# Kernel tuning notes

Measured on AMD Instinct MI355X. Metric: run time of the kernel, lower is better.

The kernel has to match this reference:

```python
import jax, jax.numpy as jnp
import numpy as np

H = 16; W = 16; C_IN = 32; RNN_IN = 64; HID = 128; OUT = 512; B = 512


def _upsample_bilinear_ac(x, oh, ow):
    """Bilinear upsample with align_corners=True (matches nn.UpsamplingBilinear2d). x: (B,C,h,w)."""
    h, w = x.shape[2], x.shape[3]
    ys = (jnp.arange(oh, dtype=jnp.float32) * (h - 1) / (oh - 1))
    y0 = jnp.floor(ys).astype(jnp.int32)
    y1 = jnp.minimum(y0 + 1, h - 1)
    wy = (ys - y0.astype(jnp.float32))[None, None, :, None]
    xs = (jnp.arange(ow, dtype=jnp.float32) * (w - 1) / (ow - 1))
    x0 = jnp.floor(xs).astype(jnp.int32)
    x1 = jnp.minimum(x0 + 1, w - 1)
    wx = (xs - x0.astype(jnp.float32))[None, None, None, :]
    rows = x[:, :, y0, :] * (1.0 - wy) + x[:, :, y1, :] * wy  # (B,C,oh,w)
    out = rows[:, :, :, x0] * (1.0 - wx) + rows[:, :, :, x1] * wx  # (B,C,oh,ow)
    return out


def setup_inputs() -> dict:
    key = jax.random.key(0)
    ks = jax.random.split(key, 8)
    def winit(k, shape, fan_in):
        return jax.random.normal(k, shape, jnp.float32) / np.float32(np.sqrt(fan_in))
    return {
        "x": jax.random.normal(ks[0], (B, C_IN, H, W), jnp.float32),
        "h0": jax.random.normal(ks[1], (B, HID), jnp.float32),
        "W_in": winit(ks[2], (RNN_IN, C_IN), C_IN),
        "b_in": jnp.zeros((RNN_IN,), jnp.float32),
        "W_ih": winit(ks[3], (HID, RNN_IN), RNN_IN),
        "b_ih": jnp.zeros((HID,), jnp.float32),
        "W_hh": winit(ks[4], (HID, HID), HID),
        "b_hh": jnp.zeros((HID,), jnp.float32),
        "W_out": winit(ks[5], (OUT, HID), HID),
        "b_out": jnp.zeros((OUT,), jnp.float32),
    }


def reference(x, h0, W_in, b_in, W_ih, b_ih, W_hh, b_hh, W_out, b_out):
    b = x.shape[0]
    # (B,C,H,W) -> (B,L,C), L = H*W raster order
    x_seq = x.transpose(0, 2, 3, 1).reshape(b, H * W, C_IN)
    proj = x_seq @ W_in.T + b_in                      # (B,L,RNN_IN)
    pre = proj @ W_ih.T + b_ih                        # (B,L,HID), input part of RNNCell precomputed

    def step(h, p_t):
        h_new = jnp.tanh(p_t + h @ W_hh.T + b_hh)
        return h_new, h_new

    _, hs = jax.lax.scan(step, h0, pre.transpose(1, 0, 2))  # (L,B,HID)
    hs_map = hs.reshape(H, W, b, HID).transpose(2, 3, 0, 1)  # (B,HID,H,W)
    up = _upsample_bilinear_ac(hs_map, 2 * H, 2 * W)         # (B,HID,32,32)
    act = up * jnp.clip(up + 3.0, 0.0, 6.0) * (1.0 / 6.0)    # hardswish
    pooled = act.mean(axis=(2, 3))                           # (B,HID)
    return pooled @ W_out.T + b_out
```

## Files before the change

### kernel.cpp

```cpp
#include <hip/hip_runtime.h>

#define L 256
#define BATCH 512
#define CIN 32
#define HIDN 128
#define OUTN 512

typedef _Float16 f16x8 __attribute__((ext_vector_type(8)));
typedef float f32x4 __attribute__((ext_vector_type(4)));

#define MFMA16(a, b, c) __builtin_amdgcn_mfma_f32_16x16x32_f16(a, b, c, 0, 0, 0)

static __device__ __forceinline__ unsigned short f16b(_Float16 h) {
    unsigned short u; __builtin_memcpy(&u, &h, 2); return u;
}


__global__ __launch_bounds__(256) void prep_kernel(
    const float* __restrict__ x,
    const float* __restrict__ W_in, const float* __restrict__ b_in,
    const float* __restrict__ W_ih, const float* __restrict__ b_ih,
    const float* __restrict__ b_hh, const float* __restrict__ Whh,
    unsigned short* __restrict__ Wh, unsigned short* __restrict__ Wl,
    unsigned short* __restrict__ Wch, unsigned short* __restrict__ Wcl,
    float* __restrict__ bpre, unsigned short* __restrict__ xT)
{
    const int tid = threadIdx.x;

    if (blockIdx.x != 0) {
        const int bb = blockIdx.x - 1;
        __shared__ float tile[32][16][33];
        const int wv = tid >> 6, l = tid & 63;
        const int wn = l >> 2, wc0 = (l & 3) * 8;
        for (int tc = 0; tc < 8; ++tc) {
#pragma unroll
            for (int r = 0; r < 16; ++r) {
                int i = tid + r * 256;
                int nn = i >> 8, cc = (i >> 3) & 31, tq = i & 7;
                float4 v = *(const float4*)(
                    x + ((size_t)(bb * 16 + nn) * CIN + cc) * L + tc * 32 + tq * 4);
                int cs = cc ^ ((tq & 3) << 3);
                tile[tq * 4 + 0][nn][cs] = v.x;
                tile[tq * 4 + 1][nn][cs] = v.y;
                tile[tq * 4 + 2][nn][cs] = v.z;
                tile[tq * 4 + 3][nn][cs] = v.w;
            }
            __syncthreads();
#pragma unroll
            for (int it = 0; it < 8; ++it) {
                int tl = wv + it * 4;
                int swz = ((tl >> 2) & 3) << 3;
                const float* src = &tile[tl][wn][wc0 ^ swz];
                unsigned short o[8];
#pragma unroll
                for (int k = 0; k < 8; ++k) o[k] = f16b((_Float16)src[k]);
                *(uint4*)(xT + ((size_t)(tc * 32 + tl) * BATCH + bb * 16 + wn) * CIN + wc0)
                    = *(uint4*)o;
            }
            __syncthreads();
        }
        return;
    }

    __shared__ float win[64 * CIN];
    for (int i = tid; i < 64 * CIN; i += 256) win[i] = W_in[i];
    __syncthreads();
    if (tid < 128) {
        const int j = tid;
        float acc[CIN];
#pragma unroll
        for (int c = 0; c < CIN; ++c) acc[c] = 0.f;
        float bs = b_ih[j] + b_hh[j];
        for (int m = 0; m < 64; ++m) {
            float w = W_ih[j * 64 + m];
            bs += w * b_in[m];
#pragma unroll
            for (int c = 0; c < CIN; ++c) acc[c] += w * win[m * CIN + c];
        }
        bpre[j] = bs;
#pragma unroll
        for (int c = 0; c < CIN; ++c) {
            _Float16 h = (_Float16)acc[c];
            _Float16 lo = (_Float16)(acc[c] - (float)h);
            Wch[j * CIN + c] = f16b(h);
            Wcl[j * CIN + c] = f16b(lo);
        }
    } else {
        const int j = tid - 128;
        for (int k = 0; k < HIDN; k += 4) {
            float4 v = *(const float4*)(Whh + j * HIDN + k);
            float vv[4] = {v.x, v.y, v.z, v.w};
#pragma unroll
            for (int u = 0; u < 4; ++u) {
                _Float16 h = (_Float16)vv[u];
                _Float16 lo = (_Float16)(vv[u] - (float)h);
                Wh[j * HIDN + k + u] = f16b(h);
                Wl[j * HIDN + k + u] = f16b(lo);
            }
        }
    }
}

__global__ __launch_bounds__(512, 1) void rnn_kernel(
    const float* __restrict__ h0,
    const unsigned short* __restrict__ Wh, const unsigned short* __restrict__ Wl,
    const unsigned short* __restrict__ Wch, const unsigned short* __restrict__ Wcl,
    const float* __restrict__ bpre, const unsigned short* __restrict__ xT,
    unsigned short* __restrict__ hs)
{
    const int tid = threadIdx.x;
    const int bb = blockIdx.x;
    const int lane = tid & 63;
    const int w = tid >> 6;
    const int n = lane & 15;
    const int q = lane >> 4;

    __shared__ unsigned short hbuf[2][16][HIDN];

    f16x8 Ah[4], Al[4], Axh, Axl;
    const int jr = w * 16 + n;
#pragma unroll
    for (int kc = 0; kc < 4; ++kc) {
        Ah[kc] = *(const f16x8*)(Wh + jr * HIDN + kc * 32 + q * 8);
        Al[kc] = *(const f16x8*)(Wl + jr * HIDN + kc * 32 + q * 8);
    }
    Axh = *(const f16x8*)(Wch + jr * CIN + q * 8);
    Axl = *(const f16x8*)(Wcl + jr * CIN + q * 8);
    float4 bv = *(const float4*)(bpre + w * 16 + q * 4);
    f32x4 bp = (f32x4){bv.x, bv.y, bv.z, bv.w};
    const f32x4 zero4 = (f32x4){0.f, 0.f, 0.f, 0.f};

    const unsigned short* xp = xT + ((size_t)(bb * 16 + n) * CIN + q * 8);
    f16x8 xb0, xb1;
    xb0 = *(const f16x8*)(xp);

    if (tid < 256) {
        const int ni = tid >> 4, gi = tid & 15;
        const float4* src = (const float4*)(h0 + ((size_t)bb * 16 + ni) * HIDN + gi * 8);
        float4 a = src[0], b4 = src[1];
        float vv[8] = {a.x, a.y, a.z, a.w, b4.x, b4.y, b4.z, b4.w};
        unsigned short o[8];
#pragma unroll
        for (int i = 0; i < 8; ++i) o[i] = f16b((_Float16)vv[i]);
        *(uint4*)&hbuf[0][ni][(gi ^ (ni & 7)) * 8] = *(uint4*)o;
    }
    __syncthreads();

    unsigned short* hsp = hs + ((size_t)bb * 16 + n) * HIDN + w * 16 + q * 4;
    const int G = (w * 2 + (q >> 1)) ^ (n & 7);
    const int sw = n & 7;

#define STEP(T, IN, OUT, XCUR, XNEXT)                                          \
    {                                                                          \
        XNEXT = *(const f16x8*)(xp + (size_t)((T) + 1) * (BATCH * CIN));       \
        f16x8 Bh0 = *(const f16x8*)&hbuf[IN][n][((0 + q) ^ sw) * 8];           \
        f16x8 Bh1 = *(const f16x8*)&hbuf[IN][n][((4 + q) ^ sw) * 8];           \
        f16x8 Bh2 = *(const f16x8*)&hbuf[IN][n][((8 + q) ^ sw) * 8];           \
        f16x8 Bh3 = *(const f16x8*)&hbuf[IN][n][((12 + q) ^ sw) * 8];          \
        f32x4 c0 = MFMA16(Axh, XCUR, bp);                                      \
        f32x4 c2 = MFMA16(Axl, XCUR, zero4);                                   \
        c0 = MFMA16(Ah[0], Bh0, c0);                                           \
        c2 = MFMA16(Al[0], Bh0, c2);                                           \
        f32x4 c1 = MFMA16(Ah[1], Bh1, zero4);                                  \
        f32x4 c3 = MFMA16(Al[1], Bh1, zero4);                                  \
        c0 = MFMA16(Ah[2], Bh2, c0);                                           \
        c2 = MFMA16(Al[2], Bh2, c2);                                           \
        c1 = MFMA16(Ah[3], Bh3, c1);                                           \
        c3 = MFMA16(Al[3], Bh3, c3);                                           \
        f32x4 acc = (c0 + c1) + (c2 + c3);                                     \
        unsigned short o[4];                                                   \
        for (int r = 0; r < 4; ++r) {                                          \
            float e = __expf(2.f * acc[r]);                                    \
            float hv = 1.f - 2.f * __builtin_amdgcn_rcpf(e + 1.f);             \
            o[r] = f16b((_Float16)hv);                                         \
        }                                                                      \
        uint2 pk; __builtin_memcpy(&pk, o, 8);                                 \
        *(uint2*)&hbuf[OUT][n][G * 8 + (q & 1) * 4] = pk;                      \
        *(uint2*)(hsp + (size_t)(T) * (BATCH * HIDN)) = pk;                    \
        asm volatile("" ::: "memory");                                         \
        __builtin_amdgcn_s_waitcnt(0xC07F);               \
        __builtin_amdgcn_s_barrier();                                          \
        asm volatile("" ::: "memory");                                         \
    }

    for (int t = 0; t < L; t += 2) {
        STEP(t,     0, 1, xb0, xb1);
        STEP(t + 1, 1, 0, xb1, xb0);
    }
#undef STEP
}

__global__ __launch_bounds__(256) void pool_out_kernel(
    const unsigned short* __restrict__ hs, const float* __restrict__ W_out,
    const float* __restrict__ b_out, float* __restrict__ out)
{
    const int b = blockIdx.x, tid = threadIdx.x;
    __shared__ unsigned short m[L][HIDN];
    __shared__ float ps[2][HIDN];
    __shared__ float pooled_s[HIDN];

#pragma unroll
    for (int it = 0; it < 16; ++it) {
        int i = tid + it * 256;
        int t = i >> 4, g = i & 15;
        *(uint4*)&m[t][g * 8] =
            *(const uint4*)(hs + (size_t)t * (BATCH * HIDN) + b * HIDN + g * 8);
    }
    __syncthreads();

    const int jo = tid & 127, sub = tid >> 7;
    float acc = 0.f;
    for (int oy = sub * 16; oy < sub * 16 + 16; ++oy) {
        float ysf = oy * (15.f / 31.f);
        int y0 = (int)ysf; float wy = ysf - (float)y0; int y1 = min(y0 + 1, 15);
        float rb[16];
#pragma unroll
        for (int sx = 0; sx < 16; ++sx) {
            float v0 = (float)*(const _Float16*)&m[y0 * 16 + sx][jo];
            float v1 = (float)*(const _Float16*)&m[y1 * 16 + sx][jo];
            rb[sx] = v0 + wy * (v1 - v0);
        }
#pragma unroll
        for (int ox = 0; ox < 32; ++ox) {
            float xsf = ox * (15.f / 31.f);
            int x0 = (int)xsf; float wx = xsf - (float)x0; int x1 = min(x0 + 1, 15);
            float v = rb[x0] + wx * (rb[x1] - rb[x0]);
            float t6 = fminf(fmaxf(v + 3.f, 0.f), 6.f);
            acc += v * t6;
        }
    }
    ps[sub][jo] = acc;
    __syncthreads();
    if (tid < 128) pooled_s[tid] = (ps[0][tid] + ps[1][tid]) * (1.f / 6144.f);
    __syncthreads();

    for (int o = tid; o < OUTN; o += 256) {
        float a = b_out[o];
#pragma unroll 8
        for (int k = 0; k < HIDN; k += 4) {
            float4 wv = *(const float4*)(W_out + o * HIDN + k);
            float4 pv = *(const float4*)&pooled_s[k];
            a += wv.x * pv.x + wv.y * pv.y + wv.z * pv.z + wv.w * pv.w;
        }
        out[b * OUTN + o] = a;
    }
}

extern "C" void kernel_launch(void* const* d_in, const int* in_sizes, int n_in,
                              void* d_out, int out_size, void* d_ws, size_t ws_size,
                              hipStream_t stream)
{
    const float* x     = (const float*)d_in[0];
    const float* h0    = (const float*)d_in[1];
    const float* W_in  = (const float*)d_in[2];
    const float* b_in  = (const float*)d_in[3];
    const float* W_ih  = (const float*)d_in[4];
    const float* b_ih  = (const float*)d_in[5];
    const float* W_hh  = (const float*)d_in[6];
    const float* b_hh  = (const float*)d_in[7];
    const float* W_out = (const float*)d_in[8];
    const float* b_out = (const float*)d_in[9];
    float* out = (float*)d_out;

    char* wsb = (char*)d_ws;
    unsigned short* Wh  = (unsigned short*)(wsb);
    unsigned short* Wl  = (unsigned short*)(wsb + 32768);
    unsigned short* Wch = (unsigned short*)(wsb + 65536);
    unsigned short* Wcl = (unsigned short*)(wsb + 73728);
    float* bpre         = (float*)(wsb + 81920);
    unsigned short* hsb = (unsigned short*)(wsb + 98304);
    unsigned short* xT  = (unsigned short*)(wsb + 33652736);

    prep_kernel<<<33, 256, 0, stream>>>(x, W_in, b_in, W_ih, b_ih, b_hh, W_hh,
                                        Wh, Wl, Wch, Wcl, bpre, xT);
    rnn_kernel<<<32, 512, 0, stream>>>(h0, Wh, Wl, Wch, Wcl, bpre, xT, hsb);
    pool_out_kernel<<<512, 256, 0, stream>>>(hsb, W_out, b_out, out);
}
```

Before: 245.1 us.

## Prefetch x in 8-step batches in RNN loop and split prep transpose

The recurrent kernel now loads input projections for 8 timesteps at once into register arrays, double-buffered, instead of one step ahead, and unrolls 16 steps per loop iteration. The prep kernel splits each batch-block's transpose across two blocks and stages W_ih and b_in in shared memory for the weight fold. The aim is to hide global-load latency on the serial recurrence and shorten the prep kernel, at the cost of more registers. The per-step vmcnt(0) wait may still force the batched loads to complete early.

```diff
diff --git a/kernel.cpp b/kernel.cpp
--- a/kernel.cpp
+++ b/kernel.cpp
@@ -28,11 +28,13 @@
     const int tid = threadIdx.x;
 
     if (blockIdx.x != 0) {
-        const int bb = blockIdx.x - 1;
+        const int idx0 = blockIdx.x - 1;
+        const int bb = idx0 & 31;
+        const int half = idx0 >> 5;
         __shared__ float tile[32][16][33];
         const int wv = tid >> 6, l = tid & 63;
         const int wn = l >> 2, wc0 = (l & 3) * 8;
-        for (int tc = 0; tc < 8; ++tc) {
+        for (int tc = half * 4; tc < half * 4 + 4; ++tc) {
 #pragma unroll
             for (int r = 0; r < 16; ++r) {
                 int i = tid + r * 256;
@@ -63,7 +65,11 @@
     }
 
     __shared__ float win[64 * CIN];
+    __shared__ float wih[128 * 64];
+    __shared__ float binS[64];
     for (int i = tid; i < 64 * CIN; i += 256) win[i] = W_in[i];
+    for (int i = tid; i < 128 * 64; i += 256) wih[i] = W_ih[i];
+    if (tid < 64) binS[tid] = b_in[tid];
     __syncthreads();
     if (tid < 128) {
         const int j = tid;
@@ -72,8 +78,8 @@
         for (int c = 0; c < CIN; ++c) acc[c] = 0.f;
         float bs = b_ih[j] + b_hh[j];
         for (int m = 0; m < 64; ++m) {
-            float w = W_ih[j * 64 + m];
-            bs += w * b_in[m];
+            float w = wih[j * 64 + m];
+            bs += w * binS[m];
 #pragma unroll
             for (int c = 0; c < CIN; ++c) acc[c] += w * win[m * CIN + c];
         }
@@ -117,6 +123,17 @@
 
     __shared__ unsigned short hbuf[2][16][HIDN];
 
+    const unsigned short* xq = xT + ((size_t)(bb * 16 + n) * CIN + q * 8);
+    f16x8 xa[8], xb[8];
+#define ISSUE8(ARR, TB)                                                        \
+    do {                                                                       \
+        _Pragma("unroll")                                                      \
+        for (int ii = 0; ii < 8; ++ii)                                         \
+            ARR[ii] = *(const f16x8*)(xq + (size_t)((TB) + ii) * (BATCH * CIN)); \
+    } while (0)
+    ISSUE8(xa, 0);
+    ISSUE8(xb, 8);
+
     f16x8 Ah[4], Al[4], Axh, Axl;
     const int jr = w * 16 + n;
 #pragma unroll
@@ -129,10 +146,6 @@
     float4 bv = *(const float4*)(bpre + w * 16 + q * 4);
     f32x4 bp = (f32x4){bv.x, bv.y, bv.z, bv.w};
     const f32x4 zero4 = (f32x4){0.f, 0.f, 0.f, 0.f};
-
-    const unsigned short* xp = xT + ((size_t)(bb * 16 + n) * CIN + q * 8);
-    f16x8 xb0, xb1;
-    xb0 = *(const f16x8*)(xp);
 
     if (tid < 256) {
         const int ni = tid >> 4, gi = tid & 15;
@@ -150,14 +163,14 @@
     const int G = (w * 2 + (q >> 1)) ^ (n & 7);
     const int sw = n & 7;
 
-#define STEP(T, IN, OUT, XCUR, XNEXT)                                          \
+#define STEP(K, XCUR)                                                          \
     {                                                                          \
-        XNEXT = *(const f16x8*)(xp + (size_t)((T) + 1) * (BATCH * CIN));       \
+        const int IN = (K) & 1, OUT = IN ^ 1;                                  \
         f16x8 Bh0 = *(const f16x8*)&hbuf[IN][n][((0 + q) ^ sw) * 8];           \
         f16x8 Bh1 = *(const f16x8*)&hbuf[IN][n][((4 + q) ^ sw) * 8];           \
         f16x8 Bh2 = *(const f16x8*)&hbuf[IN][n][((8 + q) ^ sw) * 8];           \
         f16x8 Bh3 = *(const f16x8*)&hbuf[IN][n][((12 + q) ^ sw) * 8];          \
-        f32x4 c0 = MFMA16(Axh, XCUR, bp);                                      \
+        f32x4 c0 = MFMA16(Axh, XCUR, bp);            \
         f32x4 c2 = MFMA16(Axl, XCUR, zero4);                                   \
         c0 = MFMA16(Ah[0], Bh0, c0);                                           \
         c2 = MFMA16(Al[0], Bh0, c2);                                           \
@@ -176,18 +189,24 @@
         }                                                                      \
         uint2 pk; __builtin_memcpy(&pk, o, 8);                                 \
         *(uint2*)&hbuf[OUT][n][G * 8 + (q & 1) * 4] = pk;                      \
-        *(uint2*)(hsp + (size_t)(T) * (BATCH * HIDN)) = pk;                    \
+        *(uint2*)(hsp + (K) * (BATCH * HIDN)) = pk;                            \
         asm volatile("" ::: "memory");                                         \
-        __builtin_amdgcn_s_waitcnt(0xC07F);               \
+        __builtin_amdgcn_s_waitcnt(0xC07F);    \
         __builtin_amdgcn_s_barrier();                                          \
         asm volatile("" ::: "memory");                                         \
     }
 
-    for (int t = 0; t < L; t += 2) {
-        STEP(t,     0, 1, xb0, xb1);
-        STEP(t + 1, 1, 0, xb1, xb0);
+    for (int tc = 0; tc < 16; ++tc) {
+        STEP(0, xa[0]); STEP(1, xa[1]); STEP(2, xa[2]); STEP(3, xa[3]);
+        STEP(4, xa[4]); STEP(5, xa[5]); STEP(6, xa[6]); STEP(7, xa[7]);
+        if (tc < 15) ISSUE8(xa, tc * 16 + 16);
+        STEP(8, xb[0]); STEP(9, xb[1]); STEP(10, xb[2]); STEP(11, xb[3]);
+        STEP(12, xb[4]); STEP(13, xb[5]); STEP(14, xb[6]); STEP(15, xb[7]);
+        if (tc < 15) ISSUE8(xb, tc * 16 + 24);
+        hsp += 16 * (BATCH * HIDN);
     }
 #undef STEP
+#undef ISSUE8
 }
 
 __global__ __launch_bounds__(256) void pool_out_kernel(
@@ -271,7 +290,7 @@
     unsigned short* hsb = (unsigned short*)(wsb + 98304);
     unsigned short* xT  = (unsigned short*)(wsb + 33652736);
 
-    prep_kernel<<<33, 256, 0, stream>>>(x, W_in, b_in, W_ih, b_ih, b_hh, W_hh,
+    prep_kernel<<<65, 256, 0, stream>>>(x, W_in, b_in, W_ih, b_ih, b_hh, W_hh,
                                         Wh, Wl, Wch, Wcl, bpre, xT);
     rnn_kernel<<<32, 512, 0, stream>>>(h0, Wh, Wl, Wch, Wcl, bpre, xT, hsb);
     pool_out_kernel<<<512, 256, 0, stream>>>(hsb, W_out, b_out, out);
```

After: 230.1 us. -6.1%, faster.
